# Kernel optimization log

Measured on AMD Instinct MI355X. Metric: run time of the kernel, lower is better.

The kernel has to match this reference:

```python
import jax, jax.numpy as jnp
import numpy as np
import math

B = 16384
INPUT = 2048
HIDDEN = 2048
PROJ = 1024


def setup_inputs() -> dict:
    key = jax.random.key(0)
    ks = jax.random.split(key, 20)
    stdv = 1.0 / math.sqrt(PROJ)
    u = lambda k, shape: jax.random.uniform(k, shape, jnp.float32, -stdv, stdv)
    return {
        "x_t": jax.random.normal(ks[0], (B, INPUT), jnp.float32),
        "h_t": jax.random.normal(ks[1], (B, PROJ), jnp.float32),
        "c_t": jax.random.normal(ks[2], (B, HIDDEN), jnp.float32),
        "weight_if_x": u(ks[3], (INPUT, 2 * HIDDEN)),
        "weight_if_h": u(ks[4], (PROJ, 2 * HIDDEN)),
        "weight_if_c": u(ks[5], (HIDDEN, 2 * HIDDEN)),
        "bias_i": u(ks[6], (HIDDEN,)),
        "bias_f": u(ks[7], (HIDDEN,)),
        "weight_c_x": u(ks[8], (INPUT, HIDDEN)),
        "weight_c_h": u(ks[9], (PROJ, HIDDEN)),
        "bias_c": u(ks[10], (HIDDEN,)),
        "weight_o_x": u(ks[11], (INPUT, PROJ)),
        "weight_o_h": u(ks[12], (PROJ, PROJ)),
        "weight_o_c": u(ks[13], (HIDDEN, PROJ)),
        "bias_o": u(ks[14], (PROJ,)),
        "weight_r_proj": u(ks[15], (HIDDEN, PROJ)),
        "weight_r_x": u(ks[16], (INPUT, PROJ)),
    }


def reference(x_t, h_t, c_t, weight_if_x, weight_if_h, weight_if_c, bias_i, bias_f,
              weight_c_x, weight_c_h, bias_c, weight_o_x, weight_o_h, weight_o_c,
              bias_o, weight_r_proj, weight_r_x):
    # input/forget gates with peephole on c_t: [B, 2*HIDDEN]
    if_gates = x_t @ weight_if_x + h_t @ weight_if_h + c_t @ weight_if_c
    ingate, forgetgate = jnp.split(if_gates, 2, axis=-1)
    ingate = jax.nn.sigmoid(ingate + bias_i)
    forgetgate = jax.nn.sigmoid(forgetgate + bias_f)
    cellgate = jnp.tanh(x_t @ weight_c_x + h_t @ weight_c_h + bias_c)
    c_new = forgetgate * c_t + ingate * cellgate
    # output gate peeps at new cell state
    outgate = jax.nn.sigmoid(x_t @ weight_o_x + h_t @ weight_o_h + c_new @ weight_o_c + bias_o)
    r_t = jnp.tanh(c_new)
    m_t = r_t @ weight_r_proj
    # input_size != proj_size -> project x for the residual connection
    h_new = outgate * (m_t + x_t @ weight_r_x)
    return (h_new, c_new)
```

## Files before the change

### kernel.cpp

```cpp
#include <hip/hip_runtime.h>
#include <hip/hip_bf16.h>
#include <math.h>

typedef unsigned short u16;
typedef __bf16 bf16x8_t __attribute__((ext_vector_type(8)));
typedef float  f32x4_t  __attribute__((ext_vector_type(4)));
typedef float  f32x8_t  __attribute__((ext_vector_type(8)));
typedef u16    u16x4_t  __attribute__((ext_vector_type(4)));
typedef u16    u16x8_t  __attribute__((ext_vector_type(8)));

__device__ __forceinline__ u16 f2b(float f) {
  unsigned u = __builtin_bit_cast(unsigned, f);
  u += 0x7fffu + ((u >> 16) & 1u);
  return (u16)(u >> 16);
}
__device__ __forceinline__ float b2f(u16 h) {
  unsigned u = ((unsigned)h) << 16;
  return __builtin_bit_cast(float, u);
}
__device__ __forceinline__ float sigm_(float x) { return 1.0f / (1.0f + __expf(-x)); }
__device__ __forceinline__ float tanh_(float x) { return 1.0f - 2.0f / (__expf(2.0f * x) + 1.0f); }

__device__ __forceinline__ void gload16(const void* g, void* l) {
  __builtin_amdgcn_global_load_lds(
      (__attribute__((address_space(1))) void*)(g),
      (__attribute__((address_space(3))) void*)(l), 16, 0, 0);
}


__global__ void pack_act_kernel(const float* __restrict__ x, const float* __restrict__ h,
                                const float* __restrict__ c, u16* __restrict__ A1p) {
  int mb = blockIdx.x, kt = blockIdx.y, t = threadIdx.x;
  const float* src; int C, ccol;
  if (kt < 64)      { src = x; C = 2048; ccol = kt * 32; }
  else if (kt < 96) { src = h; C = 1024; ccol = (kt - 64) * 32; }
  else              { src = c; C = 2048; ccol = (kt - 96) * 32; }
  const float* s = src + (long)(mb * 256 + t) * C + ccol;
  u16* d = A1p + ((long)(mb * 160 + kt)) * 8192 + t * 8;
#pragma unroll
  for (int p = 0; p < 4; ++p) {
    f32x8_t v = *(const f32x8_t*)(s + p * 8);
    u16x8_t o;
#pragma unroll
    for (int r = 0; r < 8; ++r) o[r] = f2b(v[r]);
    *(u16x8_t*)(d + p * 2048) = o;
  }
}

__global__ void pack_w1_kernel(const float* __restrict__ w_if_x, const float* __restrict__ w_if_h,
                               const float* __restrict__ w_if_c, const float* __restrict__ w_c_x,
                               const float* __restrict__ w_c_h,  const float* __restrict__ w_o_x,
                               const float* __restrict__ w_o_h,  const float* __restrict__ w_r_x,
                               u16* __restrict__ W1tp) {
  int nb = blockIdx.x, kt = blockIdx.y, t = threadIdx.x;
  int n0g = nb * 256;
  const float* src; int N, nl, kl;
  if (n0g < 4096) {
    N = 4096; nl = n0g;
    if (kt < 64)      { src = w_if_x; kl = kt * 32; }
    else if (kt < 96) { src = w_if_h; kl = (kt - 64) * 32; }
    else              { src = w_if_c; kl = (kt - 96) * 32; }
  } else if (n0g < 6144) {
    N = 2048; nl = n0g - 4096;
    if (kt < 64)      { src = w_c_x; kl = kt * 32; }
    else if (kt < 96) { src = w_c_h; kl = (kt - 64) * 32; }
    else return;
  } else if (n0g < 7168) {
    N = 1024; nl = n0g - 6144;
    if (kt < 64)      { src = w_o_x; kl = kt * 32; }
    else if (kt < 96) { src = w_o_h; kl = (kt - 64) * 32; }
    else return;
  } else {
    N = 1024; nl = n0g - 7168;
    if (kt < 64)      { src = w_r_x; kl = kt * 32; }
    else return;
  }
  int n = nl + t;
  float tmp[32];
#pragma unroll
  for (int kk = 0; kk < 32; ++kk)
    tmp[kk] = src[(long)(kl + kk) * N + n];
  u16* d = W1tp + ((long)(nb * 160 + kt)) * 8192 + t * 8;
#pragma unroll
  for (int p = 0; p < 4; ++p) {
    u16x8_t o;
#pragma unroll
    for (int r = 0; r < 8; ++r) o[r] = f2b(tmp[p * 8 + r]);
    *(u16x8_t*)(d + p * 2048) = o;
  }
}

__global__ void pack_w2_kernel(const float* __restrict__ w_o_c,
                               const float* __restrict__ w_r_proj, u16* __restrict__ W2q) {
  int cg = blockIdx.x, kt = blockIdx.y, t = threadIdx.x;
  const float* src; int kl;
  if (kt < 64) { src = w_o_c;    kl = kt * 32; }
  else         { src = w_r_proj; kl = (kt - 64) * 32; }
  int n = cg * 128 + t;
  float tmp[32];
#pragma unroll
  for (int kk = 0; kk < 32; ++kk)
    tmp[kk] = src[(long)(kl + kk) * 1024 + n];
  u16* d = W2q + ((long)(cg * 128 + kt)) * 4096 + t * 8;
#pragma unroll
  for (int p = 0; p < 4; ++p) {
    u16x8_t o;
#pragma unroll
    for (int r = 0; r < 8; ++r) o[r] = f2b(tmp[p * 8 + r]);
    *(u16x8_t*)(d + p * 1024) = o;
  }
}

struct FragSet { bf16x8_t bv[4]; bf16x8_t av[4]; };

__global__ __launch_bounds__(512, 2) void gemm1_kernel(
    const u16* __restrict__ A, const u16* __restrict__ Bt, u16* __restrict__ Cout) {
  constexpr int KTF  = 160;
  constexpr int NCOL = 8192;
  constexpr int NBN  = 32;
  constexpr int SLOT = 16384;

  __shared__ u16 lds[4 * SLOT];

  int bid = blockIdx.x;
  int cpx = gridDim.x >> 3;
  bid = (bid & 7) * cpx + (bid >> 3);

  int mb = bid / NBN, nb = bid % NBN;
  int m0 = mb * 256, n0 = nb * 256;

  int NT = (nb < 16) ? 160 : ((nb < 28) ? 96 : 64);

  const int tid  = threadIdx.x;
  const int lane = tid & 63;
  const int wid  = tid >> 6;
  const int wr   = wid >> 2;
  const int wc   = wid & 3;
  const int hl16 = lane >> 4;
  const int l15  = lane & 15;

  const int dstg = tid * 8;
  const u16* pA = A  + ((long)(mb * KTF)) * 8192 + dstg;
  const u16* pB = Bt + ((long)(nb * KTF)) * 8192 + dstg;

#define STAGE_A(t, s) do { \
    gload16(pA + (long)(t) * 8192,        &lds[(s) * SLOT + dstg]); \
    gload16(pA + (long)(t) * 8192 + 4096, &lds[(s) * SLOT + dstg + 4096]); } while (0)
#define STAGE_B(t, s) do { \
    gload16(pB + (long)(t) * 8192,        &lds[(s) * SLOT + 8192 + dstg]); \
    gload16(pB + (long)(t) * 8192 + 4096, &lds[(s) * SLOT + 8192 + dstg + 4096]); } while (0)

  const int aoff = hl16 * 2048 + (wr * 128 + l15) * 8;
  const int boff = hl16 * 2048 + (wc * 64  + l15) * 8;

#define RD_P(S, si) do { \
    const u16* _pb = &lds[(si) * SLOT]; \
    const u16* _pc = _pb + 8192; \
    _Pragma("unroll") \
    for (int n = 0; n < 4; ++n) S.bv[n] = *(const bf16x8_t*)&_pc[boff + n * 128]; \
    _Pragma("unroll") \
    for (int m = 0; m < 4; ++m) S.av[m] = *(const bf16x8_t*)&_pb[aoff + m * 128]; } while (0)

#define ITER(TT, P, N) do { \
    const int _t = (TT); \
    const u16* _sb = &lds[(_t & 3) * SLOT]; \
    const bool _p3 = (_t + 3 < NT); \
    if (_p3) STAGE_A(_t + 3, (_t + 3) & 3); \
    bf16x8_t _aq0 = *(const bf16x8_t*)&_sb[aoff + 4 * 128]; \
    bf16x8_t _aq1 = *(const bf16x8_t*)&_sb[aoff + 5 * 128]; \
    bf16x8_t _aq2 = *(const bf16x8_t*)&_sb[aoff + 6 * 128]; \
    bf16x8_t _aq3 = *(const bf16x8_t*)&_sb[aoff + 7 * 128]; \
    __builtin_amdgcn_s_setprio(1); \
    _Pragma("unroll") \
    for (int m = 0; m < 4; ++m) \
      _Pragma("unroll") \
      for (int n = 0; n < 4; ++n) \
        acc[m][n] = __builtin_amdgcn_mfma_f32_16x16x32_bf16(P.bv[n], P.av[m], acc[m][n], 0, 0, 0); \
    __builtin_amdgcn_s_setprio(0); \
    if (_p3) STAGE_B(_t + 3, (_t + 3) & 3); \
    if (_t + 1 < NT) RD_P(N, (_t + 1) & 3); \
    __builtin_amdgcn_s_setprio(1); \
    _Pragma("unroll") \
    for (int n = 0; n < 4; ++n) { \
      acc[4][n] = __builtin_amdgcn_mfma_f32_16x16x32_bf16(P.bv[n], _aq0, acc[4][n], 0, 0, 0); \
      acc[5][n] = __builtin_amdgcn_mfma_f32_16x16x32_bf16(P.bv[n], _aq1, acc[5][n], 0, 0, 0); \
      acc[6][n] = __builtin_amdgcn_mfma_f32_16x16x32_bf16(P.bv[n], _aq2, acc[6][n], 0, 0, 0); \
      acc[7][n] = __builtin_amdgcn_mfma_f32_16x16x32_bf16(P.bv[n], _aq3, acc[7][n], 0, 0, 0); \
    } \
    __builtin_amdgcn_s_setprio(0); \
    if (_p3) asm volatile("s_waitcnt vmcnt(4)" ::: "memory"); \
    else     asm volatile("s_waitcnt vmcnt(0)" ::: "memory"); \
    __builtin_amdgcn_s_barrier(); \
  } while (0)

  f32x4_t acc[8][4];
#pragma unroll
  for (int m = 0; m < 8; ++m)
#pragma unroll
    for (int n = 0; n < 4; ++n) acc[m][n] = (f32x4_t){0.f, 0.f, 0.f, 0.f};

  STAGE_A(0, 0); STAGE_B(0, 0);
  STAGE_A(1, 1); STAGE_B(1, 1);
  STAGE_A(2, 2); STAGE_B(2, 2);
  asm volatile("s_waitcnt vmcnt(4)" ::: "memory");
  __builtin_amdgcn_s_barrier();

  FragSet FA, FB;
  RD_P(FA, 0);

  for (int t = 0; t < NT; t += 2) {
    ITER(t,     FA, FB);
    ITER(t + 1, FB, FA);
  }
#undef STAGE_A
#undef STAGE_B
#undef RD_P
#undef ITER

  const int rowm = lane & 15;
  const int col4 = (lane >> 4) * 4;
#pragma unroll
  for (int m = 0; m < 8; ++m) {
    long rg = (long)(m0 + wr * 128 + m * 16 + rowm) * NCOL;
#pragma unroll
    for (int n = 0; n < 4; ++n) {
      int cg = n0 + wc * 64 + n * 16 + col4;
      u16x4_t o;
#pragma unroll
      for (int r = 0; r < 4; ++r) o[r] = f2b(acc[m][n][r]);
      *(u16x4_t*)&Cout[rg + cg] = o;
    }
  }
}

__global__ void pass2_kernel(const u16* __restrict__ G1, const float* __restrict__ c_t,
                             const float* __restrict__ bias_i, const float* __restrict__ bias_f,
                             const float* __restrict__ bias_c,
                             float* __restrict__ c_new_out, u16* __restrict__ A2p) {
  int mb = blockIdx.x, jg = blockIdx.y, t = threadIdx.x;
  int b = mb * 256 + t;
  int j0 = jg * 32;
  const u16* row = G1 + (long)b * 8192 + j0;
  const float* cp_p = c_t + (long)b * 2048 + j0;
  float* co_p = c_new_out + (long)b * 2048 + j0;
  u16* dc = A2p + ((long)(mb * 128 + jg)) * 8192 + t * 8;
  u16* dr = dc + (long)64 * 8192;

#pragma unroll
  for (int q = 0; q < 4; ++q) {
    u16x8_t ip = *(const u16x8_t*)(row + q * 8);
    u16x8_t fp = *(const u16x8_t*)(row + 2048 + q * 8);
    u16x8_t gp = *(const u16x8_t*)(row + 4096 + q * 8);
    f32x8_t cp = *(const f32x8_t*)(cp_p + q * 8);
    f32x8_t bi = *(const f32x8_t*)(bias_i + j0 + q * 8);
    f32x8_t bf = *(const f32x8_t*)(bias_f + j0 + q * 8);
    f32x8_t bc = *(const f32x8_t*)(bias_c + j0 + q * 8);
    f32x8_t cn;
    u16x8_t cb, rb;
#pragma unroll
    for (int r = 0; r < 8; ++r) {
      float ig = sigm_(b2f(ip[r]) + bi[r]);
      float fg = sigm_(b2f(fp[r]) + bf[r]);
      float g  = tanh_(b2f(gp[r]) + bc[r]);
      float c  = fg * cp[r] + ig * g;
      cn[r] = c;
      cb[r] = f2b(c);
      rb[r] = f2b(tanh_(c));
    }
    *(f32x8_t*)(co_p + q * 8) = cn;
    *(u16x8_t*)(dc + q * 2048) = cb;
    *(u16x8_t*)(dr + q * 2048) = rb;
  }
}

__global__ __launch_bounds__(512, 2) void gemm2h_kernel(
    const u16* __restrict__ A2p, const u16* __restrict__ W2q,
    const u16* __restrict__ G1, const float* __restrict__ bias_o,
    float* __restrict__ h_out) {
  constexpr int SLOT = 12288;

  __shared__ u16 lds[3 * SLOT];

  int bid = blockIdx.x;
  int cpx = gridDim.x >> 3;
  bid = (bid & 7) * cpx + (bid >> 3);

  int mb = bid >> 3, cg = bid & 7;
  int m0 = mb * 256, c0 = cg * 128;

  const int tid  = threadIdx.x;
  const int lane = tid & 63;
  const int wid  = tid >> 6;
  const int wr   = wid >> 1;
  const int wc   = wid & 1;
  const int hl16 = lane >> 4;
  const int l15  = lane & 15;

  const int dstg = tid * 8;
  const u16* pA = A2p + ((long)(mb * 128)) * 8192 + dstg;
  const u16* pB = W2q + ((long)(cg * 128)) * 4096 + dstg;

#define STAGE2(t, s) do { \
    gload16(pA + (long)(t) * 8192,        &lds[(s) * SLOT + dstg]); \
    gload16(pA + (long)(t) * 8192 + 4096, &lds[(s) * SLOT + dstg + 4096]); \
    gload16(pB + (long)(t) * 4096,        &lds[(s) * SLOT + 8192 + dstg]); } while (0)

  const int aoff = hl16 * 2048 + (wr * 64 + l15) * 8;
  const int boff = hl16 * 1024 + (wc * 64 + l15) * 8;

  f32x4_t acc0[4][4], acc1[4][4];
#pragma unroll
  for (int m = 0; m < 4; ++m)
#pragma unroll
    for (int n = 0; n < 4; ++n) {
      acc0[m][n] = (f32x4_t){0.f, 0.f, 0.f, 0.f};
      acc1[m][n] = (f32x4_t){0.f, 0.f, 0.f, 0.f};
    }

  STAGE2(0, 0); STAGE2(1, 1);
  asm volatile("s_waitcnt vmcnt(3)" ::: "memory");
  __builtin_amdgcn_s_barrier();

  int slot = 0, s2 = 2;
  for (int t = 0; t < 128; ++t) {
    const u16* sA = &lds[slot * SLOT];
    const u16* sB = sA + 8192;
    const bool pre = (t + 2 < 128);
    if (pre) STAGE2(t + 2, s2);

    bf16x8_t wv[4], av[4];
#pragma unroll
    for (int n = 0; n < 4; ++n) wv[n] = *(const bf16x8_t*)&sB[boff + n * 128];
#pragma unroll
    for (int m = 0; m < 4; ++m) av[m] = *(const bf16x8_t*)&sA[aoff + m * 128];

    __builtin_amdgcn_s_setprio(1);
    if (t < 64) {
#pragma unroll
      for (int m = 0; m < 4; ++m)
#pragma unroll
        for (int n = 0; n < 4; ++n)
          acc0[m][n] = __builtin_amdgcn_mfma_f32_16x16x32_bf16(wv[n], av[m], acc0[m][n], 0, 0, 0);
    } else {
#pragma unroll
      for (int m = 0; m < 4; ++m)
#pragma unroll
        for (int n = 0; n < 4; ++n)
          acc1[m][n] = __builtin_amdgcn_mfma_f32_16x16x32_bf16(wv[n], av[m], acc1[m][n], 0, 0, 0);
    }
    __builtin_amdgcn_s_setprio(0);

    if (pre) asm volatile("s_waitcnt vmcnt(3)" ::: "memory");
    else     asm volatile("s_waitcnt vmcnt(0)" ::: "memory");
    __builtin_amdgcn_s_barrier();

    slot = (slot == 2) ? 0 : slot + 1;
    s2   = (s2   == 2) ? 0 : s2   + 1;
  }
#undef STAGE2

#pragma unroll
  for (int m = 0; m < 4; ++m) {
    int row = m0 + wr * 64 + m * 16 + l15;
    const u16* g1r = G1 + (long)row * 8192;
#pragma unroll
    for (int n = 0; n < 4; ++n) {
      int jb = c0 + wc * 64 + n * 16 + 4 * hl16;
      u16x4_t og = *(const u16x4_t*)(g1r + 6144 + jb);
      u16x4_t xr = *(const u16x4_t*)(g1r + 7168 + jb);
      f32x4_t bo = *(const f32x4_t*)(bias_o + jb);
      f32x4_t h;
#pragma unroll
      for (int r = 0; r < 4; ++r) {
        float ogate = sigm_(acc0[m][n][r] + b2f(og[r]) + bo[r]);
        h[r] = ogate * (acc1[m][n][r] + b2f(xr[r]));
      }
      *(f32x4_t*)&h_out[(long)row * 1024 + jb] = h;
    }
  }
}

extern "C" void kernel_launch(void* const* d_in, const int* in_sizes, int n_in,
                              void* d_out, int out_size, void* d_ws, size_t ws_size,
                              hipStream_t stream) {
  const float* x_t      = (const float*)d_in[0];
  const float* h_t      = (const float*)d_in[1];
  const float* c_t      = (const float*)d_in[2];
  const float* w_if_x   = (const float*)d_in[3];
  const float* w_if_h   = (const float*)d_in[4];
  const float* w_if_c   = (const float*)d_in[5];
  const float* bias_i   = (const float*)d_in[6];
  const float* bias_f   = (const float*)d_in[7];
  const float* w_c_x    = (const float*)d_in[8];
  const float* w_c_h    = (const float*)d_in[9];
  const float* bias_c   = (const float*)d_in[10];
  const float* w_o_x    = (const float*)d_in[11];
  const float* w_o_h    = (const float*)d_in[12];
  const float* w_o_c    = (const float*)d_in[13];
  const float* bias_o   = (const float*)d_in[14];
  const float* w_r_proj = (const float*)d_in[15];
  const float* w_r_x    = (const float*)d_in[16];

  char* ws = (char*)d_ws;
  u16* A1p  = (u16*)(ws);
  u16* W1tp = (u16*)(ws + 167772160L);
  u16* G1   = (u16*)(ws + 251658240L);
  u16* W2q  = (u16*)(ws + 520093696L);
  u16* A2p  = (u16*)(ws);

  float* h_out = (float*)d_out;
  float* c_out = h_out + 16384L * 1024L;

  pack_act_kernel<<<dim3(64, 160), 256, 0, stream>>>(x_t, h_t, c_t, A1p);
  pack_w1_kernel<<<dim3(32, 160), 256, 0, stream>>>(w_if_x, w_if_h, w_if_c, w_c_x, w_c_h,
                                                    w_o_x, w_o_h, w_r_x, W1tp);
  pack_w2_kernel<<<dim3(8, 128), 128, 0, stream>>>(w_o_c, w_r_proj, W2q);

  gemm1_kernel<<<2048, 512, 0, stream>>>(A1p, W1tp, G1);

  pass2_kernel<<<dim3(64, 64), 256, 0, stream>>>(G1, c_t, bias_i, bias_f, bias_c, c_out, A2p);

  gemm2h_kernel<<<512, 512, 0, stream>>>(A2p, W2q, G1, bias_o, h_out);
}
```

Before: 1.450 ms.

## Merge pack kernels into one launch and retile gemm2 to 128x256 blocks

Folds the three bf16 packing kernels into a single launch with a combined grid, which removes two launches and their tail gaps. The second GEMM's block tile changes from 256 rows by 128 columns to 128 rows by 256 columns. W2 is repacked with 256-column groups, and A is loaded as a half-slice of the existing 256-row packed layout. The new tile reuses each loaded A tile across more output columns, but the epilogue indexing and the wave layout (2x4 waves) must match the changed tile. Parts of the epilogue are hidden, so there is some risk of mismatch.

```diff
diff --git a/kernel.cpp b/kernel.cpp
--- a/kernel.cpp
+++ b/kernel.cpp
@@ -28,86 +28,95 @@
 }
 
 
-__global__ void pack_act_kernel(const float* __restrict__ x, const float* __restrict__ h,
-                                const float* __restrict__ c, u16* __restrict__ A1p) {
-  int mb = blockIdx.x, kt = blockIdx.y, t = threadIdx.x;
-  const float* src; int C, ccol;
-  if (kt < 64)      { src = x; C = 2048; ccol = kt * 32; }
-  else if (kt < 96) { src = h; C = 1024; ccol = (kt - 64) * 32; }
-  else              { src = c; C = 2048; ccol = (kt - 96) * 32; }
-  const float* s = src + (long)(mb * 256 + t) * C + ccol;
-  u16* d = A1p + ((long)(mb * 160 + kt)) * 8192 + t * 8;
-#pragma unroll
-  for (int p = 0; p < 4; ++p) {
-    f32x8_t v = *(const f32x8_t*)(s + p * 8);
-    u16x8_t o;
-#pragma unroll
-    for (int r = 0; r < 8; ++r) o[r] = f2b(v[r]);
-    *(u16x8_t*)(d + p * 2048) = o;
-  }
-}
-
-__global__ void pack_w1_kernel(const float* __restrict__ w_if_x, const float* __restrict__ w_if_h,
-                               const float* __restrict__ w_if_c, const float* __restrict__ w_c_x,
-                               const float* __restrict__ w_c_h,  const float* __restrict__ w_o_x,
-                               const float* __restrict__ w_o_h,  const float* __restrict__ w_r_x,
-                               u16* __restrict__ W1tp) {
-  int nb = blockIdx.x, kt = blockIdx.y, t = threadIdx.x;
-  int n0g = nb * 256;
-  const float* src; int N, nl, kl;
-  if (n0g < 4096) {
-    N = 4096; nl = n0g;
-    if (kt < 64)      { src = w_if_x; kl = kt * 32; }
-    else if (kt < 96) { src = w_if_h; kl = (kt - 64) * 32; }
-    else              { src = w_if_c; kl = (kt - 96) * 32; }
-  } else if (n0g < 6144) {
-    N = 2048; nl = n0g - 4096;
-    if (kt < 64)      { src = w_c_x; kl = kt * 32; }
-    else if (kt < 96) { src = w_c_h; kl = (kt - 64) * 32; }
-    else return;
-  } else if (n0g < 7168) {
-    N = 1024; nl = n0g - 6144;
-    if (kt < 64)      { src = w_o_x; kl = kt * 32; }
-    else if (kt < 96) { src = w_o_h; kl = (kt - 64) * 32; }
-    else return;
-  } else {
-    N = 1024; nl = n0g - 7168;
-    if (kt < 64)      { src = w_r_x; kl = kt * 32; }
-    else return;
-  }
-  int n = nl + t;
-  float tmp[32];
-#pragma unroll
-  for (int kk = 0; kk < 32; ++kk)
-    tmp[kk] = src[(long)(kl + kk) * N + n];
-  u16* d = W1tp + ((long)(nb * 160 + kt)) * 8192 + t * 8;
-#pragma unroll
-  for (int p = 0; p < 4; ++p) {
-    u16x8_t o;
-#pragma unroll
-    for (int r = 0; r < 8; ++r) o[r] = f2b(tmp[p * 8 + r]);
-    *(u16x8_t*)(d + p * 2048) = o;
-  }
-}
-
-__global__ void pack_w2_kernel(const float* __restrict__ w_o_c,
-                               const float* __restrict__ w_r_proj, u16* __restrict__ W2q) {
-  int cg = blockIdx.x, kt = blockIdx.y, t = threadIdx.x;
-  const float* src; int kl;
-  if (kt < 64) { src = w_o_c;    kl = kt * 32; }
-  else         { src = w_r_proj; kl = (kt - 64) * 32; }
-  int n = cg * 128 + t;
-  float tmp[32];
-#pragma unroll
-  for (int kk = 0; kk < 32; ++kk)
-    tmp[kk] = src[(long)(kl + kk) * 1024 + n];
-  u16* d = W2q + ((long)(cg * 128 + kt)) * 4096 + t * 8;
-#pragma unroll
-  for (int p = 0; p < 4; ++p) {
-    u16x8_t o;
-#pragma unroll
-    for (int r = 0; r < 8; ++r) o[r] = f2b(tmp[p * 8 + r]);
-    *(u16x8_t*)(d + p * 1024) = o;
+__global__ void pack_all_kernel(const float* __restrict__ x, const float* __restrict__ h,
+                                const float* __restrict__ c,
+                                const float* __restrict__ w_if_x, const float* __restrict__ w_if_h,
+                                const float* __restrict__ w_if_c, const float* __restrict__ w_c_x,
+                                const float* __restrict__ w_c_h,  const float* __restrict__ w_o_x,
+                                const float* __restrict__ w_o_h,  const float* __restrict__ w_r_x,
+                                const float* __restrict__ w_o_c,  const float* __restrict__ w_r_proj,
+                                u16* __restrict__ A1p, u16* __restrict__ W1tp,
+                                u16* __restrict__ W2q) {
+  int bx = blockIdx.x, by = blockIdx.y, t = threadIdx.x;
+
+  if (bx < 64) {
+    int mb = bx, kt = by;
+    const float* src; int C, ccol;
+    if (kt < 64)      { src = x; C = 2048; ccol = kt * 32; }
+    else if (kt < 96) { src = h; C = 1024; ccol = (kt - 64) * 32; }
+    else              { src = c; C = 2048; ccol = (kt - 96) * 32; }
+    const float* s = src + (long)(mb * 256 + t) * C + ccol;
+    u16* d = A1p + ((long)(mb * 160 + kt)) * 8192 + t * 8;
+#pragma unroll
+    for (int p = 0; p < 4; ++p) {
+      f32x8_t v = *(const f32x8_t*)(s + p * 8);
+      u16x8_t o;
+#pragma unroll
+      for (int r = 0; r < 8; ++r) o[r] = f2b(v[r]);
+      *(u16x8_t*)(d + p * 2048) = o;
+    }
+    return;
+  }
+
+  if (bx < 96) {
+    int nb = bx - 64, kt = by;
+    int n0g = nb * 256;
+    const float* src; int N, nl, kl;
+    if (n0g < 4096) {
+      N = 4096; nl = n0g;
+      if (kt < 64)      { src = w_if_x; kl = kt * 32; }
+      else if (kt < 96) { src = w_if_h; kl = (kt - 64) * 32; }
+      else              { src = w_if_c; kl = (kt - 96) * 32; }
+    } else if (n0g < 6144) {
+      N = 2048; nl = n0g - 4096;
+      if (kt < 64)      { src = w_c_x; kl = kt * 32; }
+      else if (kt < 96) { src = w_c_h; kl = (kt - 64) * 32; }
+      else return;
+    } else if (n0g < 7168) {
+      N = 1024; nl = n0g - 6144;
+      if (kt < 64)      { src = w_o_x; kl = kt * 32; }
+      else if (kt < 96) { src = w_o_h; kl = (kt - 64) * 32; }
+      else return;
+    } else {
+      N = 1024; nl = n0g - 7168;
+      if (kt < 64)      { src = w_r_x; kl = kt * 32; }
+      else return;
+    }
+    int n = nl + t;
+    float tmp[32];
+#pragma unroll
+    for (int kk = 0; kk < 32; ++kk)
+      tmp[kk] = src[(long)(kl + kk) * N + n];
+    u16* d = W1tp + ((long)(nb * 160 + kt)) * 8192 + t * 8;
+#pragma unroll
+    for (int p = 0; p < 4; ++p) {
+      u16x8_t o;
+#pragma unroll
+      for (int r = 0; r < 8; ++r) o[r] = f2b(tmp[p * 8 + r]);
+      *(u16x8_t*)(d + p * 2048) = o;
+    }
+    return;
+  }
+
+  {
+    int cg = bx - 96, kt = by;
+    if (kt >= 128) return;
+    const float* src; int kl;
+    if (kt < 64) { src = w_o_c;    kl = kt * 32; }
+    else         { src = w_r_proj; kl = (kt - 64) * 32; }
+    int n = cg * 256 + t;
+    float tmp[32];
+#pragma unroll
+    for (int kk = 0; kk < 32; ++kk)
+      tmp[kk] = src[(long)(kl + kk) * 1024 + n];
+    u16* d = W2q + ((long)(cg * 128 + kt)) * 8192 + t * 8;
+#pragma unroll
+    for (int p = 0; p < 4; ++p) {
+      u16x8_t o;
+#pragma unroll
+      for (int r = 0; r < 8; ++r) o[r] = f2b(tmp[p * 8 + r]);
+      *(u16x8_t*)(d + p * 2048) = o;
+    }
   }
 }
 
@@ -285,28 +294,29 @@
   int cpx = gridDim.x >> 3;
   bid = (bid & 7) * cpx + (bid >> 3);
 
-  int mb = bid >> 3, cg = bid & 7;
-  int m0 = mb * 256, c0 = cg * 128;
+  int rb = bid >> 2, cg = bid & 3;
+  int m0 = rb * 128, c0 = cg * 256;
 
   const int tid  = threadIdx.x;
   const int lane = tid & 63;
   const int wid  = tid >> 6;
-  const int wr   = wid >> 1;
-  const int wc   = wid & 1;
+  const int wr   = wid >> 2;
+  const int wc   = wid & 3;
   const int hl16 = lane >> 4;
   const int l15  = lane & 15;
 
+  const u16* pA = A2p + ((long)((rb >> 1) * 128)) * 8192
+                + (tid >> 7) * 2048 + (rb & 1) * 1024 + (tid & 127) * 8;
+  const u16* pB = W2q + ((long)(cg * 128)) * 8192 + tid * 8;
   const int dstg = tid * 8;
-  const u16* pA = A2p + ((long)(mb * 128)) * 8192 + dstg;
-  const u16* pB = W2q + ((long)(cg * 128)) * 4096 + dstg;
 
 #define STAGE2(t, s) do { \
     gload16(pA + (long)(t) * 8192,        &lds[(s) * SLOT + dstg]); \
-    gload16(pA + (long)(t) * 8192 + 4096, &lds[(s) * SLOT + dstg + 4096]); \
-    gload16(pB + (long)(t) * 4096,        &lds[(s) * SLOT + 8192 + dstg]); } while (0)
-
-  const int aoff = hl16 * 2048 + (wr * 64 + l15) * 8;
-  const int boff = hl16 * 1024 + (wc * 64 + l15) * 8;
+    gload16(pB + (long)(t) * 8192,        &lds[(s) * SLOT + 4096 + dstg]); \
+    gload16(pB + (long)(t) * 8192 + 4096, &lds[(s) * SLOT + 8192 + dstg]); } while (0)
+
+  const int aoff = hl16 * 1024 + (wr * 64 + l15) * 8;
+  const int boff = 4096 + hl16 * 2048 + (wc * 64 + l15) * 8;
 
   f32x4_t acc0[4][4], acc1[4][4];
 #pragma unroll
@@ -324,13 +334,12 @@
   int slot = 0, s2 = 2;
   for (int t = 0; t < 128; ++t) {
     const u16* sA = &lds[slot * SLOT];
-    const u16* sB = sA + 8192;
     const bool pre = (t + 2 < 128);
     if (pre) STAGE2(t + 2, s2);
 
     bf16x8_t wv[4], av[4];
 #pragma unroll
-    for (int n = 0; n < 4; ++n) wv[n] = *(const bf16x8_t*)&sB[boff + n * 128];
+    for (int n = 0; n < 4; ++n) wv[n] = *(const bf16x8_t*)&sA[boff + n * 128];
 #pragma unroll
     for (int m = 0; m < 4; ++m) av[m] = *(const bf16x8_t*)&sA[aoff + m * 128];
 
@@ -411,10 +420,9 @@
   float* h_out = (float*)d_out;
   float* c_out = h_out + 16384L * 1024L;
 
-  pack_act_kernel<<<dim3(64, 160), 256, 0, stream>>>(x_t, h_t, c_t, A1p);
-  pack_w1_kernel<<<dim3(32, 160), 256, 0, stream>>>(w_if_x, w_if_h, w_if_c, w_c_x, w_c_h,
-                                                    w_o_x, w_o_h, w_r_x, W1tp);
-  pack_w2_kernel<<<dim3(8, 128), 128, 0, stream>>>(w_o_c, w_r_proj, W2q);
+  pack_all_kernel<<<dim3(100, 160), 256, 0, stream>>>(
+      x_t, h_t, c_t, w_if_x, w_if_h, w_if_c, w_c_x, w_c_h,
+      w_o_x, w_o_h, w_r_x, w_o_c, w_r_proj, A1p, W1tp, W2q);
 
   gemm1_kernel<<<2048, 512, 0, stream>>>(A1p, W1tp, G1);
 
```

Result: no change. 1.448 ms (-0.1%).
